# Kernel tuning notes

Hardware: AMD Instinct MI355X
Metric: run time of the kernel (lower is better)

Reference implementation:

```python
import jax, jax.numpy as jnp
import numpy as np

B, N, H = 32, 512, 128
LN_EPS = 1e-5

def _layernorm(x):
    # LayerNorm over last dim, no affine (elementwise_affine=False)
    mu = jnp.mean(x, axis=-1, keepdims=True)
    var = jnp.var(x, axis=-1, keepdims=True)
    return (x - mu) * jax.lax.rsqrt(var + LN_EPS)

def setup_inputs() -> dict:
    key = jax.random.key(0)
    k0, k1, k2, k3 = jax.random.split(key, 4)
    s = jax.random.normal(k0, (B, N, H), dtype=jnp.float32)
    ev = jax.random.normal(k1, (B, N, N, 3), dtype=jnp.float32)
    mask = (jax.random.uniform(k2, (B, N, N, 1)) > 0.5).astype(jnp.float32)
    W1 = jax.random.normal(k3, (H, H), dtype=jnp.float32) / np.sqrt(H)
    b1 = jnp.zeros((H,), dtype=jnp.float32)
    return {"s": s, "ev": ev, "mask": mask, "W1": W1, "b1": b1}

def reference(s, ev, mask, W1, b1):
    # lin1: Linear -> LayerNorm (no affine) -> SiLU
    h = jnp.einsum('bnh,kh->bnk', s, W1) + b1          # (B, N, H)
    h = jax.nn.silu(_layernorm(h))
    # Fused CFConv: v[b,i,c,d] = sum_j mask[b,i,j] * ev[b,i,j,c] * h[b,j,d]
    mev = ev * mask                                     # (B, N, N, 3)
    v = jnp.einsum('bijc,bjd->bicd', mev, h)            # (B, N, 3, H)
    return v
```

## Files before the change

kernel.cpp:

```cpp
#include <hip/hip_runtime.h>
#include <hip/hip_bf16.h>

#define B_ 32
#define N_ 512
#define H_ 128

typedef float f32x4 __attribute__((ext_vector_type(4)));
typedef short short8 __attribute__((ext_vector_type(8)));
typedef short short4v __attribute__((ext_vector_type(4)));

static __device__ __forceinline__ float bf2f(unsigned short u) {
  union { unsigned int ui; float f; } x;
  x.ui = ((unsigned int)u) << 16;
  return x.f;
}
static __device__ __forceinline__ unsigned short f2bf(float f) {
  __hip_bfloat16 h = __float2bfloat16(f);
  return *reinterpret_cast<unsigned short*>(&h);
}

__global__ __launch_bounds__(256) void lin_ln_silu_kernel(
    const float* __restrict__ s, const float* __restrict__ W1,
    const float* __restrict__ b1, unsigned short* __restrict__ h_t) {
  __shared__ float s_sh[32 * 132];
  __shared__ unsigned short w_sh[128 * 132];
  __shared__ unsigned short ht_sh[128 * 40];
  const int t = threadIdx.x;
  const int b = blockIdx.y;
  const int n0 = blockIdx.x * 32;

#pragma unroll
  for (int r = 0; r < 16; ++r) {
    int q = t + 256 * r;
    int d = q >> 5, part = q & 31;
    float4 v = *reinterpret_cast<const float4*>(W1 + d * H_ + part * 4);
    short4v w;
    w.x = (short)f2bf(v.x); w.y = (short)f2bf(v.y);
    w.z = (short)f2bf(v.z); w.w = (short)f2bf(v.w);
    *reinterpret_cast<short4v*>(&w_sh[d * 132 + part * 4]) = w;
  }
#pragma unroll
  for (int r = 0; r < 4; ++r) {
    int q = t + 256 * r;
    int n = q >> 5, part = q & 31;
    float4 v = *reinterpret_cast<const float4*>(
        s + ((size_t)b * N_ + n0 + n) * H_ + part * 4);
    *reinterpret_cast<float4*>(&s_sh[n * 132 + part * 4]) = v;
  }
  __syncthreads();

  const int a = t & 15;
  const int g = t >> 4;
  float acc[2][8];
#pragma unroll
  for (int nn = 0; nn < 2; ++nn)
#pragma unroll
    for (int dd = 0; dd < 8; ++dd) acc[nn][dd] = 0.f;

  float bias[8];
#pragma unroll
  for (int dd = 0; dd < 8; ++dd) bias[dd] = b1[dd * 16 + a];

  for (int k = 0; k < 128; k += 4) {
    float wf[8][4];
#pragma unroll
    for (int dd = 0; dd < 8; ++dd) {
      short4v wv =
          *reinterpret_cast<const short4v*>(&w_sh[(dd * 16 + a) * 132 + k]);
      wf[dd][0] = bf2f((unsigned short)wv.x);
      wf[dd][1] = bf2f((unsigned short)wv.y);
      wf[dd][2] = bf2f((unsigned short)wv.z);
      wf[dd][3] = bf2f((unsigned short)wv.w);
    }
#pragma unroll
    for (int nn = 0; nn < 2; ++nn) {
      float4 sv =
          *reinterpret_cast<const float4*>(&s_sh[(nn * 16 + g) * 132 + k]);
#pragma unroll
      for (int dd = 0; dd < 8; ++dd) {
        acc[nn][dd] += sv.x * wf[dd][0] + sv.y * wf[dd][1] +
                       sv.z * wf[dd][2] + sv.w * wf[dd][3];
      }
    }
  }

#pragma unroll
  for (int nn = 0; nn < 2; ++nn) {
    float s1 = 0.f, s2 = 0.f;
#pragma unroll
    for (int dd = 0; dd < 8; ++dd) {
      float x = acc[nn][dd] + bias[dd];
      acc[nn][dd] = x;
      s1 += x;
      s2 += x * x;
    }
#pragma unroll
    for (int off = 8; off >= 1; off >>= 1) {
      s1 += __shfl_xor(s1, off);
      s2 += __shfl_xor(s2, off);
    }
    float mean = s1 * (1.f / 128.f);
    float var = s2 * (1.f / 128.f) - mean * mean;
    float rs = rsqrtf(var + 1e-5f);
#pragma unroll
    for (int dd = 0; dd < 8; ++dd) {
      float x = (acc[nn][dd] - mean) * rs;
      float y = x / (1.f + __expf(-x));
      ht_sh[(dd * 16 + a) * 40 + nn * 16 + g] = f2bf(y);
    }
  }
  __syncthreads();

#pragma unroll
  for (int r = 0; r < 2; ++r) {
    int q = t + 256 * r;
    int d = q >> 2, part = q & 3;
    float4 v = *reinterpret_cast<const float4*>(&ht_sh[d * 40 + part * 8]);
    *reinterpret_cast<float4*>(
        h_t + ((size_t)b * 128 + d) * 512 + n0 + part * 8) = v;
  }
}

__global__ __launch_bounds__(256, 4) void cfconv_mfma_kernel(
    const float* __restrict__ ev, const float* __restrict__ mask,
    const unsigned short* __restrict__ h_t, float* __restrict__ out) {
  __shared__ unsigned short ph[48 * 72];
  __shared__ unsigned short hh[128 * 72];
  const int t = threadIdx.x;
  const int b = blockIdx.y;
  const int i0 = blockIdx.x * 16;
  const int lane = t & 63;
  const int w = t >> 6;
  const int l15 = lane & 15;
  const int quad = lane >> 4;

  const int si = t >> 4;
  const int sj = t & 15;
  const int hd = t >> 3;
  const int hp = t & 7;
  const float* evbase =
      ev + ((size_t)(b * N_ + i0 + si)) * N_ * 3 + (size_t)sj * 12;
  const float* mbase = mask + ((size_t)(b * N_ + i0 + si)) * N_ + sj * 4;
  const unsigned short* hbase = h_t + (size_t)b * 128 * 512;

  f32x4 acc[3][2];
#pragma unroll
  for (int mt = 0; mt < 3; ++mt)
#pragma unroll
    for (int nt = 0; nt < 2; ++nt)
#pragma unroll
      for (int e = 0; e < 4; ++e) acc[mt][nt][e] = 0.f;

  float4 hvA[4], evvA[3], mkvA;
  float4 hvB[4], evvB[3], mkvB;

#define ISSUE(HV, EVV, MKV, JR)                                              \
  do {                                                                       \
    const int jn_ = (JR)*64;                                                 \
    _Pragma("unroll") for (int r2 = 0; r2 < 4; ++r2) {                       \
      int d_ = hd + 32 * r2;                                                 \
      HV[r2] = *reinterpret_cast<const float4*>(                             \
          hbase + (size_t)d_ * 512 + jn_ + hp * 8);                          \
    }                                                                        \
    _Pragma("unroll") for (int e_ = 0; e_ < 3; ++e_) {                       \
      EVV[e_] = *reinterpret_cast<const float4*>(evbase + (size_t)jn_ * 3 +  \
                                                 e_ * 4);                    \
    }                                                                        \
    MKV = *reinterpret_cast<const float4*>(mbase + jn_);                     \
  } while (0)

#define STAGE(HV, EVV, MKV)                                                  \
  do {                                                                       \
    _Pragma("unroll") for (int r2 = 0; r2 < 4; ++r2) {                       \
      int d_ = hd + 32 * r2;                                                 \
      *reinterpret_cast<float4*>(&hh[d_ * 72 + hp * 8]) = HV[r2];            \
    }                                                                        \
    float f_[12] = {EVV[0].x, EVV[0].y, EVV[0].z, EVV[0].w,                  \
                    EVV[1].x, EVV[1].y, EVV[1].z, EVV[1].w,                  \
                    EVV[2].x, EVV[2].y, EVV[2].z, EVV[2].w};                 \
    float mk_[4] = {MKV.x, MKV.y, MKV.z, MKV.w};                             \
    _Pragma("unroll") for (int c_ = 0; c_ < 3; ++c_) {                       \
      short4v pk_;                                                           \
      pk_.x = (short)f2bf(f_[0 * 3 + c_] * mk_[0]);                          \
      pk_.y = (short)f2bf(f_[1 * 3 + c_] * mk_[1]);                          \
      pk_.z = (short)f2bf(f_[2 * 3 + c_] * mk_[2]);                          \
      pk_.w = (short)f2bf(f_[3 * 3 + c_] * mk_[3]);                          \
      *reinterpret_cast<short4v*>(&ph[(c_ * 16 + si) * 72 + sj * 4]) = pk_;  \
    }                                                                        \
  } while (0)

#define COMPUTE()                                                            \
  do {                                                                       \
    _Pragma("unroll") for (int ks = 0; ks < 2; ++ks) {                       \
      short8 av[3], bv[2];                                                   \
      _Pragma("unroll") for (int mt = 0; mt < 3; ++mt) av[mt] =              \
          *reinterpret_cast<const short8*>(                                  \
              &ph[(mt * 16 + l15) * 72 + ks * 32 + quad * 8]);               \
      _Pragma("unroll") for (int nt = 0; nt < 2; ++nt) {                     \
        int d_ = w * 32 + nt * 16 + l15;                                     \
        bv[nt] = *reinterpret_cast<const short8*>(                           \
            &hh[d_ * 72 + ks * 32 + quad * 8]);                              \
      }                                                                      \
      _Pragma("unroll") for (int mt = 0; mt < 3; ++mt)                       \
          _Pragma("unroll") for (int nt = 0; nt < 2; ++nt) acc[mt][nt] =     \
          __builtin_amdgcn_mfma_f32_16x16x32_bf16(av[mt], bv[nt],            \
                                                  acc[mt][nt], 0, 0, 0);     \
    }                                                                        \
  } while (0)

#define SYNC_LGKM()                          \
  do {                                       \
    __builtin_amdgcn_sched_barrier(0);       \
    asm volatile("s_waitcnt lgkmcnt(0)");    \
    __builtin_amdgcn_s_barrier();            \
    __builtin_amdgcn_sched_barrier(0);       \
  } while (0)

  ISSUE(hvA, evvA, mkvA, 0);
  ISSUE(hvB, evvB, mkvB, 1);

#pragma unroll
  for (int rr = 0; rr < 4; ++rr) {
    SYNC_LGKM();
    STAGE(hvA, evvA, mkvA);
    SYNC_LGKM();
    if (rr < 3) ISSUE(hvA, evvA, mkvA, 2 * rr + 2);
    COMPUTE();

    SYNC_LGKM();
    STAGE(hvB, evvB, mkvB);
    SYNC_LGKM();
    if (rr < 3) ISSUE(hvB, evvB, mkvB, 2 * rr + 3);
    COMPUTE();
  }

#undef ISSUE
#undef STAGE
#undef COMPUTE
#undef SYNC_LGKM

#pragma unroll
  for (int mt = 0; mt < 3; ++mt) {
#pragma unroll
    for (int nt = 0; nt < 2; ++nt) {
      int d = w * 32 + nt * 16 + l15;
#pragma unroll
      for (int r = 0; r < 4; ++r) {
        int i = i0 + quad * 4 + r;
        out[(((size_t)b * N_ + i) * 3 + mt) * H_ + d] = acc[mt][nt][r];
      }
    }
  }
}

extern "C" void kernel_launch(void* const* d_in, const int* in_sizes, int n_in,
                              void* d_out, int out_size, void* d_ws,
                              size_t ws_size, hipStream_t stream) {
  const float* s = (const float*)d_in[0];
  const float* ev = (const float*)d_in[1];
  const float* mask = (const float*)d_in[2];
  const float* W1 = (const float*)d_in[3];
  const float* b1 = (const float*)d_in[4];
  float* out = (float*)d_out;
  unsigned short* h_t = (unsigned short*)d_ws;

  lin_ln_silu_kernel<<<dim3(N_ / 32, B_), 256, 0, stream>>>(s, W1, b1, h_t);
  cfconv_mfma_kernel<<<dim3(N_ / 16, B_), 256, 0, stream>>>(ev, mask, h_t, out);
}
```

Baseline: 211.6 us.

## Use inline-asm global loads with explicit vmcnt waits for staggered prefetch

```diff
diff --git a/kernel.cpp b/kernel.cpp
--- a/kernel.cpp
+++ b/kernel.cpp
@@ -151,61 +151,73 @@
 #pragma unroll
       for (int e = 0; e < 4; ++e) acc[mt][nt][e] = 0.f;
 
-  float4 hvA[4], evvA[3], mkvA;
-  float4 hvB[4], evvB[3], mkvB;
-
-#define ISSUE(HV, EVV, MKV, JR)                                              \
-  do {                                                                       \
-    const int jn_ = (JR)*64;                                                 \
-    _Pragma("unroll") for (int r2 = 0; r2 < 4; ++r2) {                       \
-      int d_ = hd + 32 * r2;                                                 \
-      HV[r2] = *reinterpret_cast<const float4*>(                             \
-          hbase + (size_t)d_ * 512 + jn_ + hp * 8);                          \
-    }                                                                        \
-    _Pragma("unroll") for (int e_ = 0; e_ < 3; ++e_) {                       \
-      EVV[e_] = *reinterpret_cast<const float4*>(evbase + (size_t)jn_ * 3 +  \
-                                                 e_ * 4);                    \
-    }                                                                        \
-    MKV = *reinterpret_cast<const float4*>(mbase + jn_);                     \
-  } while (0)
-
-#define STAGE(HV, EVV, MKV)                                                  \
-  do {                                                                       \
-    _Pragma("unroll") for (int r2 = 0; r2 < 4; ++r2) {                       \
-      int d_ = hd + 32 * r2;                                                 \
-      *reinterpret_cast<float4*>(&hh[d_ * 72 + hp * 8]) = HV[r2];            \
-    }                                                                        \
-    float f_[12] = {EVV[0].x, EVV[0].y, EVV[0].z, EVV[0].w,                  \
-                    EVV[1].x, EVV[1].y, EVV[1].z, EVV[1].w,                  \
-                    EVV[2].x, EVV[2].y, EVV[2].z, EVV[2].w};                 \
-    float mk_[4] = {MKV.x, MKV.y, MKV.z, MKV.w};                             \
-    _Pragma("unroll") for (int c_ = 0; c_ < 3; ++c_) {                       \
-      short4v pk_;                                                           \
-      pk_.x = (short)f2bf(f_[0 * 3 + c_] * mk_[0]);                          \
-      pk_.y = (short)f2bf(f_[1 * 3 + c_] * mk_[1]);                          \
-      pk_.z = (short)f2bf(f_[2 * 3 + c_] * mk_[2]);                          \
-      pk_.w = (short)f2bf(f_[3 * 3 + c_] * mk_[3]);                          \
-      *reinterpret_cast<short4v*>(&ph[(c_ * 16 + si) * 72 + sj * 4]) = pk_;  \
-    }                                                                        \
-  } while (0)
-
-#define COMPUTE()                                                            \
-  do {                                                                       \
-    _Pragma("unroll") for (int ks = 0; ks < 2; ++ks) {                       \
-      short8 av[3], bv[2];                                                   \
-      _Pragma("unroll") for (int mt = 0; mt < 3; ++mt) av[mt] =              \
-          *reinterpret_cast<const short8*>(                                  \
-              &ph[(mt * 16 + l15) * 72 + ks * 32 + quad * 8]);               \
-      _Pragma("unroll") for (int nt = 0; nt < 2; ++nt) {                     \
-        int d_ = w * 32 + nt * 16 + l15;                                     \
-        bv[nt] = *reinterpret_cast<const short8*>(                           \
-            &hh[d_ * 72 + ks * 32 + quad * 8]);                              \
-      }                                                                      \
-      _Pragma("unroll") for (int mt = 0; mt < 3; ++mt)                       \
-          _Pragma("unroll") for (int nt = 0; nt < 2; ++nt) acc[mt][nt] =     \
-          __builtin_amdgcn_mfma_f32_16x16x32_bf16(av[mt], bv[nt],            \
-                                                  acc[mt][nt], 0, 0, 0);     \
-    }                                                                        \
+  f32x4 hv[4];
+  f32x4 evvA[3], evvB[3];
+  f32x4 mkvA, mkvB;
+
+#define STR2_(x) #x
+#define VMWAIT(n) asm volatile("s_waitcnt vmcnt(" STR2_(n) ")")
+
+#define ALOAD4(DST, PTR) \
+  asm volatile("global_load_dwordx4 %0, %1, off" : "=v"(DST) : "v"(PTR))
+
+#define ISSUE_HV(JR)                                                      \
+  do {                                                                    \
+    _Pragma("unroll") for (int r2_ = 0; r2_ < 4; ++r2_) {                 \
+      const unsigned short* p_ =                                          \
+          hbase + (size_t)(hd + 32 * r2_) * 512 + (JR)*64 + hp * 8;       \
+      ALOAD4(hv[r2_], p_);                                                \
+    }                                                                     \
+  } while (0)
+
+#define ISSUE_EV(EVV, MKV, JR)                                            \
+  do {                                                                    \
+    _Pragma("unroll") for (int e_ = 0; e_ < 3; ++e_) {                    \
+      const float* p_ = evbase + (size_t)(JR)*192 + e_ * 4;               \
+      ALOAD4(EVV[e_], p_);                                                \
+    }                                                                     \
+    const float* pm_ = mbase + (JR)*64;                                   \
+    ALOAD4(MKV, pm_);                                                     \
+  } while (0)
+
+#define STAGE(EVV, MKV)                                                   \
+  do {                                                                    \
+    _Pragma("unroll") for (int r2_ = 0; r2_ < 4; ++r2_) {                 \
+      *reinterpret_cast<f32x4*>(&hh[(hd + 32 * r2_) * 72 + hp * 8]) =     \
+          hv[r2_];                                                        \
+    }                                                                     \
+    float f_[12] = {EVV[0][0], EVV[0][1], EVV[0][2], EVV[0][3],           \
+                    EVV[1][0], EVV[1][1], EVV[1][2], EVV[1][3],           \
+                    EVV[2][0], EVV[2][1], EVV[2][2], EVV[2][3]};          \
+    float mk_[4] = {MKV[0], MKV[1], MKV[2], MKV[3]};                      \
+    _Pragma("unroll") for (int c_ = 0; c_ < 3; ++c_) {                    \
+      short4v pk_;                                                        \
+      pk_.x = (short)f2bf(f_[0 * 3 + c_] * mk_[0]);                       \
+      pk_.y = (short)f2bf(f_[1 * 3 + c_] * mk_[1]);                       \
+      pk_.z = (short)f2bf(f_[2 * 3 + c_] * mk_[2]);                       \
+      pk_.w = (short)f2bf(f_[3 * 3 + c_] * mk_[3]);                       \
+      *reinterpret_cast<short4v*>(&ph[(c_ * 16 + si) * 72 + sj * 4]) =    \
+          pk_;                                                            \
+    }                                                                     \
+  } while (0)
+
+#define COMPUTE()                                                         \
+  do {                                                                    \
+    _Pragma("unroll") for (int ks = 0; ks < 2; ++ks) {                    \
+      short8 av[3], bv[2];                                                \
+      _Pragma("unroll") for (int mt = 0; mt < 3; ++mt) av[mt] =           \
+          *reinterpret_cast<const short8*>(                               \
+              &ph[(mt * 16 + l15) * 72 + ks * 32 + quad * 8]);            \
+      _Pragma("unroll") for (int nt = 0; nt < 2; ++nt) {                  \
+        int d_ = w * 32 + nt * 16 + l15;                                  \
+        bv[nt] = *reinterpret_cast<const short8*>(                        \
+            &hh[d_ * 72 + ks * 32 + quad * 8]);                          \
+      }                                                                   \
+      _Pragma("unroll") for (int mt = 0; mt < 3; ++mt)                    \
+          _Pragma("unroll") for (int nt = 0; nt < 2; ++nt) acc[mt][nt] =  \
+          __builtin_amdgcn_mfma_f32_16x16x32_bf16(av[mt], bv[nt],         \
+                                                  acc[mt][nt], 0, 0, 0);  \
+    }                                                                     \
   } while (0)
 
 #define SYNC_LGKM()                          \
@@ -216,28 +228,41 @@
     __builtin_amdgcn_sched_barrier(0);       \
   } while (0)
 
-  ISSUE(hvA, evvA, mkvA, 0);
-  ISSUE(hvB, evvB, mkvB, 1);
-
-#pragma unroll
-  for (int rr = 0; rr < 4; ++rr) {
-    SYNC_LGKM();
-    STAGE(hvA, evvA, mkvA);
-    SYNC_LGKM();
-    if (rr < 3) ISSUE(hvA, evvA, mkvA, 2 * rr + 2);
-    COMPUTE();
-
-    SYNC_LGKM();
-    STAGE(hvB, evvB, mkvB);
-    SYNC_LGKM();
-    if (rr < 3) ISSUE(hvB, evvB, mkvB, 2 * rr + 3);
-    COMPUTE();
-  }
-
-#undef ISSUE
+#define ROUND(VMN, EVV, MKV, JHV, JEV)       \
+  do {                                       \
+    SYNC_LGKM();                             \
+    VMWAIT(VMN);                             \
+    __builtin_amdgcn_sched_barrier(0);       \
+    STAGE(EVV, MKV);                         \
+    SYNC_LGKM();                             \
+    if ((JHV) < 8) ISSUE_HV(JHV);            \
+    if ((JEV) < 8) ISSUE_EV(EVV, MKV, JEV);  \
+    __builtin_amdgcn_sched_barrier(0);       \
+    COMPUTE();                               \
+  } while (0)
+
+  ISSUE_HV(0);
+  ISSUE_EV(evvA, mkvA, 0);
+  ISSUE_EV(evvB, mkvB, 1);
+
+  ROUND(4, evvA, mkvA, 1, 2);
+  ROUND(4, evvB, mkvB, 2, 3);
+  ROUND(4, evvA, mkvA, 3, 4);
+  ROUND(4, evvB, mkvB, 4, 5);
+  ROUND(4, evvA, mkvA, 5, 6);
+  ROUND(4, evvB, mkvB, 6, 7);
+  ROUND(4, evvA, mkvA, 7, 8);
+  ROUND(0, evvB, mkvB, 8, 9);
+
+#undef ROUND
+#undef SYNC_LGKM
+#undef COMPUTE
 #undef STAGE
-#undef COMPUTE
-#undef SYNC_LGKM
+#undef ISSUE_EV
+#undef ISSUE_HV
+#undef ALOAD4
+#undef VMWAIT
+#undef STR2_
 
 #pragma unroll
   for (int mt = 0; mt < 3; ++mt) {
```

After: 206.8 us. 1.02x faster.
